# Kernel tuning notes

Measured on AMD Instinct MI355X. Metric: run time of the kernel, lower is better.

## Reference

```python
import jax, jax.numpy as jnp
import numpy as np

D_MODEL = 1024
NUM_HEADS = 16
D_K = D_MODEL // NUM_HEADS


def setup_inputs() -> dict:
    key = jax.random.key(0)
    ks = jax.random.split(key, 9)
    s = 1.0 / np.sqrt(D_MODEL)
    x = jax.random.normal(ks[0], (1, 4096, D_MODEL), dtype=jnp.float32)
    Wq = jax.random.uniform(ks[1], (D_MODEL, D_MODEL), jnp.float32, -s, s)
    bq = jax.random.uniform(ks[2], (D_MODEL,), jnp.float32, -s, s)
    Wk = jax.random.uniform(ks[3], (D_MODEL, D_MODEL), jnp.float32, -s, s)
    bk = jax.random.uniform(ks[4], (D_MODEL,), jnp.float32, -s, s)
    Wv = jax.random.uniform(ks[5], (D_MODEL, D_MODEL), jnp.float32, -s, s)
    bv = jax.random.uniform(ks[6], (D_MODEL,), jnp.float32, -s, s)
    Wo = jax.random.uniform(ks[7], (D_MODEL, D_MODEL), jnp.float32, -s, s)
    bo = jax.random.uniform(ks[8], (D_MODEL,), jnp.float32, -s, s)
    return {"x": x, "Wq": Wq, "bq": bq, "Wk": Wk, "bk": bk,
            "Wv": Wv, "bv": bv, "Wo": Wo, "bo": bo}


def reference(x, Wq, bq, Wk, bk, Wv, bv, Wo, bo):
    B, S, _ = x.shape
    scale = jnp.sqrt(jnp.asarray(D_K, dtype=x.dtype))
    # projections (torch Linear: y = x @ W.T + b)
    q = (x @ Wq.T + bq).reshape(B, S, NUM_HEADS, D_K).transpose(0, 2, 1, 3)
    k = (x @ Wk.T + bk).reshape(B, S, NUM_HEADS, D_K).transpose(0, 2, 1, 3)
    v = (x @ Wv.T + bv).reshape(B, S, NUM_HEADS, D_K).transpose(0, 2, 1, 3)
    # [B, H, S, S] naive scores, causal mask, softmax
    scores = jnp.einsum('bhqd,bhkd->bhqk', q, k) / scale
    causal = jnp.tril(jnp.ones((S, S), dtype=bool))
    scores = jnp.where(causal, scores, jnp.asarray(-jnp.inf, dtype=scores.dtype))
    probs = jax.nn.softmax(scores, axis=-1)
    out = jnp.einsum('bhqk,bhkd->bhqd', probs, v)
    out = out.transpose(0, 2, 1, 3).reshape(B, S, D_MODEL)
    return out @ Wo.T + bo
```

## Files before the change

kernel.cpp:

```cpp
#include <hip/hip_runtime.h>
#include <math.h>

#define SEQ 4096
#define DMODEL 1024
#define NH 16
#define DK 64
#define LDP 72

typedef __bf16    bf16x8 __attribute__((ext_vector_type(8)));
typedef float     f32x4  __attribute__((ext_vector_type(4)));
typedef _Float16  h16x4  __attribute__((ext_vector_type(4)));
typedef _Float16  h16x8  __attribute__((ext_vector_type(8)));

#define GLOAD_LDS16(g, l) __builtin_amdgcn_global_load_lds(                     \
    (const __attribute__((address_space(1))) unsigned int*)(g),                 \
    (__attribute__((address_space(3))) unsigned int*)(l), 16, 0, 0)

__global__ __launch_bounds__(256)
void cvt_all(const float* __restrict__ x, const float* __restrict__ Wq,
             const float* __restrict__ Wk, const float* __restrict__ Wv,
             const float* __restrict__ Wo, __bf16* __restrict__ dst)
{
    const size_t M1 = 1u << 20;
    const size_t e = ((size_t)blockIdx.x * 256 + threadIdx.x) * 8;
    const float* src; size_t off;
    if      (e < 4*M1) { src = x;  off = e;        }
    else if (e < 5*M1) { src = Wq; off = e - 4*M1; }
    else if (e < 6*M1) { src = Wk; off = e - 5*M1; }
    else if (e < 7*M1) { src = Wv; off = e - 6*M1; }
    else               { src = Wo; off = e - 7*M1; }
    const float4 f0 = *reinterpret_cast<const float4*>(&src[off]);
    const float4 f1 = *reinterpret_cast<const float4*>(&src[off + 4]);
    bf16x8 pk;
    pk[0]=(__bf16)f0.x; pk[1]=(__bf16)f0.y; pk[2]=(__bf16)f0.z; pk[3]=(__bf16)f0.w;
    pk[4]=(__bf16)f1.x; pk[5]=(__bf16)f1.y; pk[6]=(__bf16)f1.z; pk[7]=(__bf16)f1.w;
    *reinterpret_cast<bf16x8*>(&dst[e]) = pk;
}

__device__ __forceinline__ void gemm_core128(const __bf16* __restrict__ A,
                                             const __bf16* __restrict__ W,
                                             int m0, int n0, int t,
                                             __bf16* AsF, __bf16* BsF,
                                             f32x4 acc[4][4])
{
    const int w = t >> 6, lane = t & 63, l15 = lane & 15, quad = lane >> 4;
    const int wm = (w & 1) * 64, wn = (w >> 1) * 64;
    const int lr = lane >> 3, lc = lane & 7;
    for (int k0 = 0; k0 < DMODEL; k0 += 64) {
        __syncthreads();
        #pragma unroll
        for (int p = 0; p < 4; ++p) {
            const int n = w*4 + p;
            const int r = n*8 + lr;
            const int cl = lc ^ (r & 7);
            GLOAD_LDS16(&A[(size_t)(m0 + r) * DMODEL + k0 + cl*8], &AsF[n*512]);
            GLOAD_LDS16(&W[(size_t)(n0 + r) * DMODEL + k0 + cl*8], &BsF[n*512]);
        }
        __syncthreads();
        #pragma unroll
        for (int kb = 0; kb < 2; ++kb) {
            const int phys = ((kb*4 + quad) ^ (l15 & 7)) * 8;
            bf16x8 af[4], bfr[4];
            #pragma unroll
            for (int i = 0; i < 4; ++i) {
                af[i]  = *reinterpret_cast<const bf16x8*>(&AsF[(wm + i*16 + l15)*64 + phys]);
                bfr[i] = *reinterpret_cast<const bf16x8*>(&BsF[(wn + i*16 + l15)*64 + phys]);
            }
            #pragma unroll
            for (int ms = 0; ms < 4; ++ms)
                #pragma unroll
                for (int ns = 0; ns < 4; ++ns)
                    acc[ms][ns] = __builtin_amdgcn_mfma_f32_16x16x32_bf16(af[ms], bfr[ns], acc[ms][ns], 0, 0, 0);
        }
    }
}

__global__ __launch_bounds__(256, 3)
void gemm_qkv(const __bf16* __restrict__ xb, const __bf16* __restrict__ Wcat,
              const float* __restrict__ bq, const float* __restrict__ bk,
              const float* __restrict__ bv,
              _Float16* __restrict__ Qh, _Float16* __restrict__ Kh, _Float16* __restrict__ Vth)
{
    __shared__ __bf16 AsF[128*64];
    __shared__ __bf16 BsF[128*64];
    const int t = threadIdx.x;
    const int n0g = blockIdx.x * 128;
    const int m0  = blockIdx.y * 128;
    const int which = n0g >> 10;
    const int n_in  = n0g & 1023;

    f32x4 acc[4][4] = {};
    gemm_core128(xb, Wcat, m0, n0g, t, AsF, BsF, acc);

    const int w = t >> 6, lane = t & 63, l15 = lane & 15, quad = lane >> 4;
    const int wm = (w & 1) * 64, wn = (w >> 1) * 64;
    const float* bias = (which == 0) ? bq : (which == 1) ? bk : bv;
    float br[4];
    #pragma unroll
    for (int ns = 0; ns < 4; ++ns) br[ns] = bias[n_in + wn + ns*16 + l15];

    if (which == 2) {
        #pragma unroll
        for (int ms = 0; ms < 4; ++ms)
            #pragma unroll
            for (int ns = 0; ns < 4; ++ns) {
                h16x4 pk;
                #pragma unroll
                for (int rg = 0; rg < 4; ++rg) pk[rg] = (_Float16)(acc[ms][ns][rg] + br[ns]);
                *reinterpret_cast<h16x4*>(
                    &Vth[(size_t)(n_in + wn + ns*16 + l15) * SEQ + m0 + wm + ms*16 + quad*4]) = pk;
            }
    } else {
        const float s = (which == 0) ? 0.1803368787f : 1.0f;
        _Float16* C = (which == 0) ? Qh : Kh;
        #pragma unroll
        for (int ms = 0; ms < 4; ++ms)
            #pragma unroll
            for (int ns = 0; ns < 4; ++ns)
                #pragma unroll
                for (int rg = 0; rg < 4; ++rg)
                    C[(size_t)(m0 + wm + ms*16 + quad*4 + rg) * DMODEL + n_in + wn + ns*16 + l15] =
                        (_Float16)((acc[ms][ns][rg] + br[ns]) * s);
    }
}

__device__ __forceinline__ void gemm_core64(const __bf16* __restrict__ A,
                                            const __bf16* __restrict__ W,
                                            int m0, int n0, int t,
                                            __bf16* AsF, __bf16* BsF,
                                            f32x4 acc[2][4])
{
    const int w = t >> 6, lane = t & 63, l15 = lane & 15, quad = lane >> 4;
    const int lr = lane >> 3, lc = lane & 7;
    for (int k0 = 0; k0 < DMODEL; k0 += 64) {
        __syncthreads();
        #pragma unroll
        for (int p = 0; p < 4; ++p) {
            const int n = w*4 + p;
            const int r = n*8 + lr;
            const int cl = lc ^ (r & 7);
            GLOAD_LDS16(&A[(size_t)(m0 + r) * DMODEL + k0 + cl*8], &AsF[n*512]);
        }
        #pragma unroll
        for (int p = 0; p < 2; ++p) {
            const int n = w*2 + p;
            const int r = n*8 + lr;
            const int cl = lc ^ (r & 7);
            GLOAD_LDS16(&W[(size_t)(n0 + r) * DMODEL + k0 + cl*8], &BsF[n*512]);
        }
        __syncthreads();
        #pragma unroll
        for (int kb = 0; kb < 2; ++kb) {
            const int phys = ((kb*4 + quad) ^ (l15 & 7)) * 8;
            bf16x8 af0 = *reinterpret_cast<const bf16x8*>(&AsF[(w*32 + l15)*64 + phys]);
            bf16x8 af1 = *reinterpret_cast<const bf16x8*>(&AsF[(w*32 + 16 + l15)*64 + phys]);
            #pragma unroll
            for (int ns = 0; ns < 4; ++ns) {
                const bf16x8 bfr = *reinterpret_cast<const bf16x8*>(&BsF[(ns*16 + l15)*64 + phys]);
                acc[0][ns] = __builtin_amdgcn_mfma_f32_16x16x32_bf16(af0, bfr, acc[0][ns], 0, 0, 0);
                acc[1][ns] = __builtin_amdgcn_mfma_f32_16x16x32_bf16(af1, bfr, acc[1][ns], 0, 0, 0);
            }
        }
    }
}

__global__ __launch_bounds__(256, 4)
void gemm_out(const __bf16* __restrict__ Ob, const __bf16* __restrict__ Wob,
              const float* __restrict__ bo, float* __restrict__ out)
{
    __shared__ __bf16 AsF[128*64];
    __shared__ __bf16 BsF[64*64];
    const int t = threadIdx.x;
    const int n0 = blockIdx.x * 64;
    const int m0 = blockIdx.y * 128;

    f32x4 acc[2][4] = {};
    gemm_core64(Ob, Wob, m0, n0, t, AsF, BsF, acc);

    const int lane = t & 63, l15 = lane & 15, quad = lane >> 4, w = t >> 6;
    float br[4];
    #pragma unroll
    for (int ns = 0; ns < 4; ++ns) br[ns] = bo[n0 + ns*16 + l15];
    #pragma unroll
    for (int ms = 0; ms < 2; ++ms)
        #pragma unroll
        for (int ns = 0; ns < 4; ++ns)
            #pragma unroll
            for (int rg = 0; rg < 4; ++rg)
                out[(size_t)(m0 + w*32 + ms*16 + quad*4 + rg) * DMODEL + n0 + ns*16 + l15] =
                    acc[ms][ns][rg] + br[ns];
}

__global__ __launch_bounds__(256, 6)
void attn_mfma(const _Float16* __restrict__ Q, const _Float16* __restrict__ K,
               const _Float16* __restrict__ Vt, __bf16* __restrict__ O,
               float* __restrict__ part, float* __restrict__ lpart)
{
    __shared__ _Float16 KsF[64*64];
    __shared__ _Float16 Vts[64][LDP];

    const int t = threadIdx.x;
    const int w = t >> 6;
    const int lane = t & 63, l15 = lane & 15, quad = lane >> 4;
    const int lr = lane >> 3, lc = lane & 7;
    const int h = blockIdx.y;
    const int u = blockIdx.x;
    int qt, g;
    if      (u < 32) { qt = 32 + u; g = 0; }
    else if (u < 64) { qt = 95 - u; g = 1; }
    else             { qt = 95 - u; g = 0; }
    const int tstart = g * 32;
    const int tend   = (qt < tstart + 31) ? qt : (tstart + 31);
    const int wr0 = qt*64 + w*16;

    h16x8 bq8[2];
    #pragma unroll
    for (int kb = 0; kb < 2; ++kb)
        bq8[kb] = *reinterpret_cast<const h16x8*>(
            &Q[(size_t)(wr0 + l15) * DMODEL + h*DK + kb*32 + quad*8]);

    f32x4 acc[4] = {};
    float lsum = 0.f;

    for (int tk = tstart; tk <= tend; ++tk) {
        const int j0 = tk * 64;
        __syncthreads();
        #pragma unroll
        for (int p = 0; p < 2; ++p) {
            const int idx = t + p * 256;
            const int r = idx >> 3, c = (idx & 7) * 8;
            *reinterpret_cast<h16x8*>(&Vts[r][c]) =
                *reinterpret_cast<const h16x8*>(&Vt[(size_t)(h*DK + r) * SEQ + j0 + c]);
        }
        #pragma unroll
        for (int p = 0; p < 2; ++p) {
            const int n = w*2 + p;
            const int r = n*8 + lr;
            const int cl = lc ^ (r & 7);
            GLOAD_LDS16(&K[(size_t)(j0 + r) * DMODEL + h*DK + cl*8], &KsF[n*512]);
        }
        __syncthreads();

        h16x4 ap[4];
        const bool msk = (j0 + 63 > wr0);
        const int rel = wr0 - j0 + l15;
        #pragma unroll
        for (int st = 0; st < 4; ++st) {
            f32x4 cc = {0.f, 0.f, 0.f, 0.f};
            #pragma unroll
            for (int kb = 0; kb < 2; ++kb) {
                const h16x8 ak = *reinterpret_cast<const h16x8*>(
                    &KsF[(st*16 + l15)*64 + (((kb*4 + quad) ^ (l15 & 7)))*8]);
                cc = __builtin_amdgcn_mfma_f32_16x16x32_f16(ak, bq8[kb], cc, 0, 0, 0);
            }
            #pragma unroll
            for (int rg = 0; rg < 4; ++rg) {
                float pv = exp2f(cc[rg]);
                if (msk && (st*16 + quad*4 + rg > rel)) pv = 0.f;
                lsum += pv;
                ap[st][rg] = (_Float16)pv;
            }
        }

        #pragma unroll
        for (int ds_ = 0; ds_ < 4; ++ds_) {
            #pragma unroll
            for (int st = 0; st < 4; ++st) {
                const h16x4 bv = *reinterpret_cast<const h16x4*>(
                    &Vts[ds_*16 + l15][st*16 + quad*4]);
                acc[ds_] = __builtin_amdgcn_mfma_f32_16x16x16f16(ap[st], bv, acc[ds_], 0, 0, 0);
            }
        }
    }

    float ls = lsum;
    ls += __shfl_xor(ls, 16);
    ls += __shfl_xor(ls, 32);

    if (qt < 32) {
        #pragma unroll
        for (int rg = 0; rg < 4; ++rg) {
            const float dn = __shfl(ls, quad*4 + rg);
            const float inv = 1.0f / dn;
            const size_t row = (size_t)(wr0 + quad*4 + rg) * DMODEL + h * DK;
            #pragma unroll
            for (int ds_ = 0; ds_ < 4; ++ds_)
                O[row + ds_*16 + l15] = (__bf16)(acc[ds_][rg] * inv);
        }
    } else {
        const int unit = (h*32 + (qt - 32))*2 + g;
        const size_t pb = (size_t)unit * 4096;
        #pragma unroll
        for (int rg = 0; rg < 4; ++rg) {
            const int lrow = w*16 + quad*4 + rg;
            #pragma unroll
            for (int ds_ = 0; ds_ < 4; ++ds_)
                part[pb + lrow*64 + ds_*16 + l15] = acc[ds_][rg];
        }
        if (quad == 0) lpart[unit*64 + w*16 + l15] = ls;
    }
}

__global__ __launch_bounds__(256)
void attn_combine(const float* __restrict__ part, const float* __restrict__ lpart,
                  __bf16* __restrict__ O)
{
    const int t = threadIdx.x;
    const int qtp = blockIdx.x;
    const int h = blockIdx.y;
    const int unit0 = (h*32 + qtp)*2;
    const size_t b0 = (size_t)unit0 * 4096;
    const size_t b1 = b0 + 4096;
    const int r  = t >> 2;
    const int d0 = (t & 3) * 16;

    const float l = lpart[unit0*64 + r] + lpart[(unit0 + 1)*64 + r];
    const float inv = 1.0f / l;
    const size_t grow = (size_t)((32 + qtp)*64 + r) * DMODEL + h*64 + d0;
    #pragma unroll
    for (int i = 0; i < 2; ++i) {
        bf16x8 pk;
        #pragma unroll
        for (int j = 0; j < 2; ++j) {
            const float4 p0 = *reinterpret_cast<const float4*>(&part[b0 + r*64 + d0 + i*8 + j*4]);
            const float4 p1 = *reinterpret_cast<const float4*>(&part[b1 + r*64 + d0 + i*8 + j*4]);
            pk[j*4+0] = (__bf16)((p0.x + p1.x) * inv);
            pk[j*4+1] = (__bf16)((p0.y + p1.y) * inv);
            pk[j*4+2] = (__bf16)((p0.z + p1.z) * inv);
            pk[j*4+3] = (__bf16)((p0.w + p1.w) * inv);
        }
        *reinterpret_cast<bf16x8*>(&O[grow + i*8]) = pk;
    }
}

extern "C" void kernel_launch(void* const* d_in, const int* in_sizes, int n_in,
                              void* d_out, int out_size, void* d_ws, size_t ws_size,
                              hipStream_t stream) {
    const float* x  = (const float*)d_in[0];
    const float* Wq = (const float*)d_in[1];
    const float* bq = (const float*)d_in[2];
    const float* Wk = (const float*)d_in[3];
    const float* bk = (const float*)d_in[4];
    const float* Wv = (const float*)d_in[5];
    const float* bv = (const float*)d_in[6];
    const float* Wo = (const float*)d_in[7];
    const float* bo = (const float*)d_in[8];
    float* out = (float*)d_out;

    const size_t M1 = 1u << 20;
    __bf16* base = (__bf16*)d_ws;
    __bf16*    xb   = base;
    __bf16*    Wcat = base + 4*M1;
    __bf16*    Wob  = base + 7*M1;
    _Float16*  Qh   = (_Float16*)(base + 8*M1);
    _Float16*  Kh   = (_Float16*)(base + 12*M1);
    _Float16*  Vth  = (_Float16*)(base + 16*M1);
    __bf16*    Ob   = base + 20*M1;
    float*     lpart = (float*)(base + 24*M1);
    float*     part  = out;

    cvt_all<<<4096, 256, 0, stream>>>(x, Wq, Wk, Wv, Wo, base);
    gemm_qkv<<<dim3(24, 32), 256, 0, stream>>>(xb, Wcat, bq, bk, bv, Qh, Kh, Vth);
    attn_mfma<<<dim3(96, NH), 256, 0, stream>>>(Qh, Kh, Vth, Ob, part, lpart);
    attn_combine<<<dim3(32, NH), 256, 0, stream>>>(part, lpart, Ob);
    gemm_out<<<dim3(16, 32), 256, 0, stream>>>(Ob, Wob, bo, out);
}
```

Before: 239.8 us.

## Process two query tiles per attention block and stage Q/K epilogue through LDS

The attention kernel now handles 128 query rows per block (two 64-row sub-tiles per warp), so each K/V tile loaded into shared memory feeds twice as many MFMAs, halving K/V traffic. The split-K scheduling, partial buffers and combine kernel are reindexed to the 128-row granularity, and launch bounds drop to 3 blocks per SU to make room for the extra registers. Separately, the Q/K epilogue of the QKV GEMM writes through an LDS tile so global stores become 16-byte row-contiguous instead of scattered 2-byte writes. The costs are fewer, larger attention blocks and lower occupancy, which may worsen load balance.

```diff
diff --git a/kernel.cpp b/kernel.cpp
--- a/kernel.cpp
+++ b/kernel.cpp
@@ -81,8 +81,9 @@
               const float* __restrict__ bv,
               _Float16* __restrict__ Qh, _Float16* __restrict__ Kh, _Float16* __restrict__ Vth)
 {
-    __shared__ __bf16 AsF[128*64];
-    __shared__ __bf16 BsF[128*64];
+    __shared__ __bf16 SM[4*64*LDP];
+    __bf16* AsF = SM;
+    __bf16* BsF = SM + 8192;
     const int t = threadIdx.x;
     const int n0g = blockIdx.x * 128;
     const int m0  = blockIdx.y * 128;
@@ -113,14 +114,24 @@
     } else {
         const float s = (which == 0) ? 0.1803368787f : 1.0f;
         _Float16* C = (which == 0) ? Qh : Kh;
+        __syncthreads();
+        _Float16* tile = (_Float16*)SM + w * 64 * LDP;
         #pragma unroll
         for (int ms = 0; ms < 4; ++ms)
             #pragma unroll
             for (int ns = 0; ns < 4; ++ns)
                 #pragma unroll
                 for (int rg = 0; rg < 4; ++rg)
-                    C[(size_t)(m0 + wm + ms*16 + quad*4 + rg) * DMODEL + n_in + wn + ns*16 + l15] =
+                    tile[(ms*16 + quad*4 + rg) * LDP + ns*16 + l15] =
                         (_Float16)((acc[ms][ns][rg] + br[ns]) * s);
+        asm volatile("s_waitcnt lgkmcnt(0)" ::: "memory");
+        const int er = lane >> 3, ec = (lane & 7) * 8;
+        #pragma unroll
+        for (int p = 0; p < 8; ++p) {
+            const h16x8 v = *reinterpret_cast<const h16x8*>(&tile[(er + p*8) * LDP + ec]);
+            *reinterpret_cast<h16x8*>(
+                &C[(size_t)(m0 + wm + er + p*8) * DMODEL + n_in + wn + ec]) = v;
+        }
     }
 }
 
@@ -191,7 +202,7 @@
                     acc[ms][ns][rg] + br[ns];
 }
 
-__global__ __launch_bounds__(256, 6)
+__global__ __launch_bounds__(256, 3)
 void attn_mfma(const _Float16* __restrict__ Q, const _Float16* __restrict__ K,
                const _Float16* __restrict__ Vt, __bf16* __restrict__ O,
                float* __restrict__ part, float* __restrict__ lpart)
@@ -206,21 +217,26 @@
     const int h = blockIdx.y;
     const int u = blockIdx.x;
     int qt, g;
-    if      (u < 32) { qt = 32 + u; g = 0; }
-    else if (u < 64) { qt = 95 - u; g = 1; }
-    else             { qt = 95 - u; g = 0; }
+    if      (u < 16) { qt = 16 + u; g = 0; }
+    else if (u < 32) { qt = u;      g = 1; }
+    else             { qt = 47 - u; g = 0; }
     const int tstart = g * 32;
-    const int tend   = (qt < tstart + 31) ? qt : (tstart + 31);
-    const int wr0 = qt*64 + w*16;
-
-    h16x8 bq8[2];
-    #pragma unroll
-    for (int kb = 0; kb < 2; ++kb)
-        bq8[kb] = *reinterpret_cast<const h16x8*>(
-            &Q[(size_t)(wr0 + l15) * DMODEL + h*DK + kb*32 + quad*8]);
-
-    f32x4 acc[4] = {};
-    float lsum = 0.f;
+    const int tlast  = 2*qt + 1;
+    const int tend   = (tlast < tstart + 31) ? tlast : (tstart + 31);
+    const int s0 = qt*128 + w*16;
+    const int s1 = s0 + 64;
+
+    h16x8 bq8[2][2];
+    #pragma unroll
+    for (int kb = 0; kb < 2; ++kb) {
+        bq8[0][kb] = *reinterpret_cast<const h16x8*>(
+            &Q[(size_t)(s0 + l15) * DMODEL + h*DK + kb*32 + quad*8]);
+        bq8[1][kb] = *reinterpret_cast<const h16x8*>(
+            &Q[(size_t)(s1 + l15) * DMODEL + h*DK + kb*32 + quad*8]);
+    }
+
+    f32x4 acc[2][4] = {};
+    float lsum[2] = {0.f, 0.f};
 
     for (int tk = tstart; tk <= tend; ++tk) {
         const int j0 = tk * 64;
@@ -241,24 +257,42 @@
         }
         __syncthreads();
 
-        h16x4 ap[4];
-        const bool msk = (j0 + 63 > wr0);
-        const int rel = wr0 - j0 + l15;
+        const bool act0 = (j0 <= s0 + 15);
+        const bool msk0 = (j0 + 63 > s0);
+        const bool msk1 = (j0 + 63 > s1);
+        const int rel0 = s0 - j0 + l15;
+        const int rel1 = s1 - j0 + l15;
+
+        h16x4 ap[2][4];
         #pragma unroll
         for (int st = 0; st < 4; ++st) {
-            f32x4 cc = {0.f, 0.f, 0.f, 0.f};
-            #pragma unroll
-            for (int kb = 0; kb < 2; ++kb) {
-                const h16x8 ak = *reinterpret_cast<const h16x8*>(
-                    &KsF[(st*16 + l15)*64 + (((kb*4 + quad) ^ (l15 & 7)))*8]);
-                cc = __builtin_amdgcn_mfma_f32_16x16x32_f16(ak, bq8[kb], cc, 0, 0, 0);
-            }
-            #pragma unroll
-            for (int rg = 0; rg < 4; ++rg) {
-                float pv = exp2f(cc[rg]);
-                if (msk && (st*16 + quad*4 + rg > rel)) pv = 0.f;
-                lsum += pv;
-                ap[st][rg] = (_Float16)pv;
+            const h16x8 ak0 = *reinterpret_cast<const h16x8*>(
+                &KsF[(st*16 + l15)*64 + ((quad ^ (l15 & 7)))*8]);
+            const h16x8 ak1 = *reinterpret_cast<const h16x8*>(
+                &KsF[(st*16 + l15)*64 + (((4 + quad) ^ (l15 & 7)))*8]);
+            {
+                f32x4 cc = {0.f, 0.f, 0.f, 0.f};
+                cc = __builtin_amdgcn_mfma_f32_16x16x32_f16(ak0, bq8[1][0], cc, 0, 0, 0);
+                cc = __builtin_amdgcn_mfma_f32_16x16x32_f16(ak1, bq8[1][1], cc, 0, 0, 0);
+                #pragma unroll
+                for (int rg = 0; rg < 4; ++rg) {
+                    float pv = exp2f(cc[rg]);
+                    if (msk1 && (st*16 + quad*4 + rg > rel1)) pv = 0.f;
+                    lsum[1] += pv;
+                    ap[1][st][rg] = (_Float16)pv;
+                }
+            }
+            if (act0) {
+                f32x4 cc = {0.f, 0.f, 0.f, 0.f};
+                cc = __builtin_amdgcn_mfma_f32_16x16x32_f16(ak0, bq8[0][0], cc, 0, 0, 0);
+                cc = __builtin_amdgcn_mfma_f32_16x16x32_f16(ak1, bq8[0][1], cc, 0, 0, 0);
+                #pragma unroll
+                for (int rg = 0; rg < 4; ++rg) {
+                    float pv = exp2f(cc[rg]);
+                    if (msk0 && (st*16 + quad*4 + rg > rel0)) pv = 0.f;
+                    lsum[0] += pv;
+                    ap[0][st][rg] = (_Float16)pv;
+                }
             }
         }
 
@@ -268,36 +302,50 @@
             for (int st = 0; st < 4; ++st) {
                 const h16x4 bv = *reinterpret_cast<const h16x4*>(
                     &Vts[ds_*16 + l15][st*16 + quad*4]);
-                acc[ds_] = __builtin_amdgcn_mfma_f32_16x16x16f16(ap[st], bv, acc[ds_], 0, 0, 0);
-            }
-        }
-    }
-
-    float ls = lsum;
-    ls += __shfl_xor(ls, 16);
-    ls += __shfl_xor(ls, 32);
-
-    if (qt < 32) {
-        #pragma unroll
-        for (int rg = 0; rg < 4; ++rg) {
-            const float dn = __shfl(ls, quad*4 + rg);
-            const float inv = 1.0f / dn;
-            const size_t row = (size_t)(wr0 + quad*4 + rg) * DMODEL + h * DK;
-            #pragma unroll
-            for (int ds_ = 0; ds_ < 4; ++ds_)
-                O[row + ds_*16 + l15] = (__bf16)(acc[ds_][rg] * inv);
+                acc[1][ds_] = __builtin_amdgcn_mfma_f32_16x16x16f16(ap[1][st], bv, acc[1][ds_], 0, 0, 0);
+                if (act0)
+                    acc[0][ds_] = __builtin_amdgcn_mfma_f32_16x16x16f16(ap[0][st], bv, acc[0][ds_], 0, 0, 0);
+            }
+        }
+    }
+
+    float ls[2];
+    #pragma unroll
+    for (int s = 0; s < 2; ++s) {
+        float v = lsum[s];
+        v += __shfl_xor(v, 16);
+        v += __shfl_xor(v, 32);
+        ls[s] = v;
+    }
+
+    if (qt < 16) {
+        #pragma unroll
+        for (int s = 0; s < 2; ++s) {
+            const int base = s ? s1 : s0;
+            #pragma unroll
+            for (int rg = 0; rg < 4; ++rg) {
+                const float dn = __shfl(ls[s], quad*4 + rg);
+                const float inv = 1.0f / dn;
+                const size_t row = (size_t)(base + quad*4 + rg) * DMODEL + h * DK;
+                #pragma unroll
+                for (int ds_ = 0; ds_ < 4; ++ds_)
+                    O[row + ds_*16 + l15] = (__bf16)(acc[s][ds_][rg] * inv);
+            }
         }
     } else {
-        const int unit = (h*32 + (qt - 32))*2 + g;
-        const size_t pb = (size_t)unit * 4096;
-        #pragma unroll
-        for (int rg = 0; rg < 4; ++rg) {
-            const int lrow = w*16 + quad*4 + rg;
-            #pragma unroll
-            for (int ds_ = 0; ds_ < 4; ++ds_)
-                part[pb + lrow*64 + ds_*16 + l15] = acc[ds_][rg];
-        }
-        if (quad == 0) lpart[unit*64 + w*16 + l15] = ls;
+        const int unit = (h*16 + (qt - 16))*2 + g;
+        const size_t pb = (size_t)unit * 8192;
+        #pragma unroll
+        for (int s = 0; s < 2; ++s) {
+            #pragma unroll
+            for (int rg = 0; rg < 4; ++rg) {
+                const int lrow = s*64 + w*16 + quad*4 + rg;
+                #pragma unroll
+                for (int ds_ = 0; ds_ < 4; ++ds_)
+                    part[pb + lrow*64 + ds_*16 + l15] = acc[s][ds_][rg];
+            }
+            if (quad == 0) lpart[unit*128 + s*64 + w*16 + l15] = ls[s];
+        }
     }
 }
 
@@ -308,17 +356,17 @@
     const int t = threadIdx.x;
     const int qtp = blockIdx.x;
     const int h = blockIdx.y;
-    const int unit0 = (h*32 + qtp)*2;
-    const size_t b0 = (size_t)unit0 * 4096;
-    const size_t b1 = b0 + 4096;
-    const int r  = t >> 2;
-    const int d0 = (t & 3) * 16;
-
-    const float l = lpart[unit0*64 + r] + lpart[(unit0 + 1)*64 + r];
+    const int u0 = (h*16 + qtp)*2;
+    const size_t b0 = (size_t)u0 * 8192;
+    const size_t b1 = b0 + 8192;
+    const int r  = t >> 1;
+    const int d0 = (t & 1) * 32;
+
+    const float l = lpart[u0*128 + r] + lpart[(u0 + 1)*128 + r];
     const float inv = 1.0f / l;
-    const size_t grow = (size_t)((32 + qtp)*64 + r) * DMODEL + h*64 + d0;
-    #pragma unroll
-    for (int i = 0; i < 2; ++i) {
+    const size_t grow = (size_t)((16 + qtp)*128 + r) * DMODEL + h*64 + d0;
+    #pragma unroll
+    for (int i = 0; i < 4; ++i) {
         bf16x8 pk;
         #pragma unroll
         for (int j = 0; j < 2; ++j) {
@@ -361,7 +409,7 @@
 
     cvt_all<<<4096, 256, 0, stream>>>(x, Wq, Wk, Wv, Wo, base);
     gemm_qkv<<<dim3(24, 32), 256, 0, stream>>>(xb, Wcat, bq, bk, bv, Qh, Kh, Vth);
-    attn_mfma<<<dim3(96, NH), 256, 0, stream>>>(Qh, Kh, Vth, Ob, part, lpart);
-    attn_combine<<<dim3(32, NH), 256, 0, stream>>>(part, lpart, Ob);
+    attn_mfma<<<dim3(48, NH), 256, 0, stream>>>(Qh, Kh, Vth, Ob, part, lpart);
+    attn_combine<<<dim3(16, NH), 256, 0, stream>>>(part, lpart, Ob);
     gemm_out<<<dim3(16, 32), 256, 0, stream>>>(Ob, Wob, bo, out);
 }
```

New measurement: 221.3 us. 7.7% less time.
